# Performance work log

Hardware: AMD Instinct MI355X
Metric: run time of the kernel (lower is better)

## Reference

```python
import jax, jax.numpy as jnp
import numpy as np

RES = 200        # self.res, hard-coded in the module
MODES_OUT = 16
MODES_IN = 32
T_SEQ = 10
D_MODEL = 256
BATCH = 16


def setup_inputs() -> dict:
    key = jax.random.key(0)
    k1, k2, k3 = jax.random.split(key, 3)
    v = jax.random.normal(k1, (BATCH, T_SEQ, D_MODEL, 2, MODES_IN), dtype=jnp.float32)
    scale = 1.0 / (MODES_IN * MODES_OUT)
    # weights1 = scale * rand(T,1,1,mo,mi) cfloat; singleton dims broadcast -> store as [T,mo,mi]
    w_real = scale * jax.random.uniform(k2, (T_SEQ, MODES_OUT, MODES_IN), dtype=jnp.float32)
    w_imag = scale * jax.random.uniform(k3, (T_SEQ, MODES_OUT, MODES_IN), dtype=jnp.float32)
    return {"v": v, "w_real": w_real, "w_imag": w_imag}


def reference(v, w_real, w_imag):
    # v: [B,T,H,2,mi] -> complex x_ft = r + i*1j
    r = v[:, :, :, 0, :]  # [B,T,H,mi]
    i = v[:, :, :, 1, :]
    # einsum 'bthix,thiox->bthox' with h=i=1 in weights == broadcast complex multiply
    wr = w_real[None, :, None, :, :]  # [1,T,1,mo,mi]
    wi = w_imag[None, :, None, :, :]
    rr = r[:, :, :, None, :]          # [B,T,H,1,mi]
    ii = i[:, :, :, None, :]
    re = rr * wr - ii * wi            # [B,T,H,mo,mi] = Re(out_ft)
    im = rr * wi + ii * wr            # Im(out_ft)
    amp = jax.nn.relu(jnp.sqrt(re * re + im * im))  # relu(|out_ft|)
    ph = jnp.arctan2(im, re)                          # angle(out_ft)
    # cosine reconstruction grid: theta[o,x] = 2*pi*f_o*x, f from fftfreq(res, d=1/(res-1))
    x_res = jnp.linspace(0.0, 1.0, RES).astype(jnp.float32)
    dx = x_res[1] - x_res[0]
    freqs = jnp.fft.fftfreq(RES, d=dx)[:MODES_OUT].astype(jnp.float32)  # [mo]
    theta = (2.0 * jnp.pi) * freqs[:, None] * x_res[None, :]            # [mo,res]
    # sum over mi of amp*cos(theta + ph) = cos(theta)*sum(amp*cos ph) - sin(theta)*sum(amp*sin ph)
    # (exact trig identity; avoids materializing the 6-D [B,T,H,mo,mi,res] tensor)
    C = jnp.sum(amp * jnp.cos(ph), axis=-1)  # [B,T,H,mo]
    S = jnp.sum(amp * jnp.sin(ph), axis=-1)  # [B,T,H,mo]
    out = (jnp.einsum('btho,ox->btxh', C, jnp.cos(theta))
           - jnp.einsum('btho,ox->btxh', S, jnp.sin(theta)))  # [B,T,res,H]
    return out
```

## Files before the change

kernel.cpp:

```cpp
#include <hip/hip_runtime.h>

#define B_   16
#define T_   10
#define D_   256
#define MI_  32
#define MO_  16
#define RES_ 200
#define TWO_PI 6.28318530717958647692f

#define HSLICE 32
#define NHS    (D_ / HSLICE)
#define VPAD   68
#define BT_STRIDE (2 * MO_ * D_)

using f32x4 = __attribute__((ext_vector_type(4))) float;
using v2f   = __attribute__((ext_vector_type(2))) float;

__global__ __launch_bounds__(256) void spectral_cs(
    const float* __restrict__ v,
    const float* __restrict__ w_real,
    const float* __restrict__ w_imag,
    float* __restrict__ ws)
{
    const int a    = blockIdx.x;
    const int r    = a & 7;
    const int rest = a >> 3;
    const int hs   = rest & 7;
    const int q    = rest >> 3;
    const int bt   = 8 * q + r;
    const int t    = bt % T_;

    __shared__ float s_v[HSLICE * VPAD];

    {
        const float4* gv = reinterpret_cast<const float4*>(
            v + ((size_t)bt * D_ + hs * HSLICE) * (2 * MI_));
        #pragma unroll
        for (int j = 0; j < 2; ++j) {
            const int f = threadIdx.x + 256 * j;
            const int h = f >> 4;
            const int m = (f & 15) * 4;
            *reinterpret_cast<float4*>(&s_v[h * VPAD + m]) = gv[f];
        }
    }
    __syncthreads();

    const int og  = threadIdx.x >> 5;
    const int h_l = threadIdx.x & 31;
    const int o0  = og * 2;
    const int h_g = hs * HSLICE + h_l;

    float rr[MI_], ii[MI_];
    #pragma unroll
    for (int j = 0; j < 8; ++j) {
        float4 q4 = *reinterpret_cast<const float4*>(&s_v[h_l * VPAD + 4 * j]);
        rr[4*j+0]=q4.x; rr[4*j+1]=q4.y; rr[4*j+2]=q4.z; rr[4*j+3]=q4.w;
    }
    #pragma unroll
    for (int j = 0; j < 8; ++j) {
        float4 q4 = *reinterpret_cast<const float4*>(&s_v[h_l * VPAD + 32 + 4 * j]);
        ii[4*j+0]=q4.x; ii[4*j+1]=q4.y; ii[4*j+2]=q4.z; ii[4*j+3]=q4.w;
    }

    const float* wrt = w_real + ((size_t)t * MO_ + o0) * MI_;
    const float* wit = w_imag + ((size_t)t * MO_ + o0) * MI_;

    float* wsb = ws + (size_t)bt * BT_STRIDE;
    #pragma unroll
    for (int ol = 0; ol < 2; ++ol) {
        const float4* wa = reinterpret_cast<const float4*>(wrt + ol * MI_);
        const float4* wb = reinterpret_cast<const float4*>(wit + ol * MI_);
        float c = 0.f, s = 0.f;
        #pragma unroll
        for (int mq = 0; mq < 8; ++mq) {
            float4 a4 = wa[mq];
            float4 b4 = wb[mq];
            c = fmaf(rr[4*mq+0], a4.x, c); c = fmaf(-ii[4*mq+0], b4.x, c);
            s = fmaf(rr[4*mq+0], b4.x, s); s = fmaf( ii[4*mq+0], a4.x, s);
            c = fmaf(rr[4*mq+1], a4.y, c); c = fmaf(-ii[4*mq+1], b4.y, c);
            s = fmaf(rr[4*mq+1], b4.y, s); s = fmaf( ii[4*mq+1], a4.y, s);
            c = fmaf(rr[4*mq+2], a4.z, c); c = fmaf(-ii[4*mq+2], b4.z, c);
            s = fmaf(rr[4*mq+2], b4.z, s); s = fmaf( ii[4*mq+2], a4.z, s);
            c = fmaf(rr[4*mq+3], a4.w, c); c = fmaf(-ii[4*mq+3], b4.w, c);
            s = fmaf(rr[4*mq+3], b4.w, s); s = fmaf( ii[4*mq+3], a4.w, s);
        }
        const int o = o0 + ol;
        v2f p; p.x = c; p.y = s;
        *reinterpret_cast<v2f*>(&wsb[2 * (o * D_ + h_g)]) = p;
    }
}

__global__ __launch_bounds__(256) void spectral_ift(
    const float* __restrict__ ws,
    float* __restrict__ out)
{
    const int b    = blockIdx.x;
    const int r    = b & 7;
    const int rest = b >> 3;
    const int qb   = rest & 3;
    const int q    = rest >> 2;
    const int bt   = 8 * q + r;
    const int wave = threadIdx.x >> 6;
    const int lane = threadIdx.x & 63;
    const int g    = qb * 4 + wave;
    const int h0   = lane * 4;

    __shared__ float s_cs[BT_STRIDE];

    {
        const float4* g4 = reinterpret_cast<const float4*>(
            ws + (size_t)bt * BT_STRIDE);
        float4* s4 = reinterpret_cast<float4*>(s_cs);
        #pragma unroll
        for (int i = 0; i < 8; ++i)
            s4[threadIdx.x + 256 * i] = g4[threadIdx.x + 256 * i];
    }
    __syncthreads();

    v2f CS0[MO_], CS1[MO_], CS2[MO_], CS3[MO_];
    #pragma unroll
    for (int o = 0; o < MO_; ++o) {
        float4 q0 = *reinterpret_cast<const float4*>(&s_cs[2 * (o * D_ + h0)]);
        float4 q1 = *reinterpret_cast<const float4*>(&s_cs[2 * (o * D_ + h0) + 4]);
        CS0[o].x = q0.x; CS0[o].y = q0.y;
        CS1[o].x = q0.z; CS1[o].y = q0.w;
        CS2[o].x = q1.x; CS2[o].y = q1.y;
        CS3[o].x = q1.z; CS3[o].y = q1.w;
    }

    float* ob = out + (size_t)bt * RES_ * D_;

    #pragma unroll
    for (int k = 0; k < 7; ++k) {
        const int s = g + 16 * k;
        if (s <= 100) {
            const float phi = (float)s * (TWO_PI / (float)RES_);
            float s1, c1;
            __sincosf(phi, &s1, &c1);

            v2f ab0 = {0.f, 0.f}, ab1 = {0.f, 0.f};
            v2f ab2 = {0.f, 0.f}, ab3 = {0.f, 0.f};
            v2f cs;  cs.x = 1.f; cs.y = 0.f;
            #pragma unroll
            for (int o = 0; o < MO_; ++o) {
                ab0 = __builtin_elementwise_fma(CS0[o], cs, ab0);
                ab1 = __builtin_elementwise_fma(CS1[o], cs, ab1);
                ab2 = __builtin_elementwise_fma(CS2[o], cs, ab2);
                ab3 = __builtin_elementwise_fma(CS3[o], cs, ab3);
                const float nc = fmaf(cs.x, c1, -(cs.y * s1));
                const float ns = fmaf(cs.y, c1,  (cs.x * s1));
                cs.x = nc; cs.y = ns;
            }

            const int mr = (s == 0) ? 0 : (RES_ - s);
            f32x4 lo, hi;
            lo.x = ab0.x - ab0.y; hi.x = ab0.x + ab0.y;
            lo.y = ab1.x - ab1.y; hi.y = ab1.x + ab1.y;
            lo.z = ab2.x - ab2.y; hi.z = ab2.x + ab2.y;
            lo.w = ab3.x - ab3.y; hi.w = ab3.x + ab3.y;
            __builtin_nontemporal_store(
                lo, reinterpret_cast<f32x4*>(&ob[(size_t)s  * D_ + h0]));
            __builtin_nontemporal_store(
                hi, reinterpret_cast<f32x4*>(&ob[(size_t)mr * D_ + h0]));
        }
    }
}

extern "C" void kernel_launch(void* const* d_in, const int* in_sizes, int n_in,
                              void* d_out, int out_size, void* d_ws, size_t ws_size,
                              hipStream_t stream) {
    const float* v  = (const float*)d_in[0];
    const float* wr = (const float*)d_in[1];
    const float* wi = (const float*)d_in[2];
    float* out = (float*)d_out;
    float* ws  = (float*)d_ws;

    spectral_cs <<<B_ * T_ * NHS, 256, 0, stream>>>(v, wr, wi, ws);
    spectral_ift<<<B_ * T_ * 4,   256, 0, stream>>>(ws, out);
}
```

Baseline: 21.65 us.

## Double ift block size, halve per-thread columns, split rotation recurrence into even/odd chains

The inverse-transform kernel now runs 512 threads per block, and each thread covers 2 hidden columns instead of 4. This halves the per-thread register arrays, which should allow higher occupancy. The twiddle recurrence is split into two interleaved chains that step by 2*phi, which shortens the serial dependency chain of the rotations. In exchange the global stores shrink from 16-byte to 8-byte vectors, and the rotation arithmetic is repeated per thread for fewer outputs.

```diff
diff --git a/kernel.cpp b/kernel.cpp
--- a/kernel.cpp
+++ b/kernel.cpp
@@ -90,7 +90,7 @@
     }
 }
 
-__global__ __launch_bounds__(256) void spectral_ift(
+__global__ __launch_bounds__(512, 4) void spectral_ift(
     const float* __restrict__ ws,
     float* __restrict__ out)
 {
@@ -102,8 +102,9 @@
     const int bt   = 8 * q + r;
     const int wave = threadIdx.x >> 6;
     const int lane = threadIdx.x & 63;
-    const int g    = qb * 4 + wave;
-    const int h0   = lane * 4;
+    const int strm = qb * 4 + (wave >> 1);
+    const int half = wave & 1;
+    const int h0   = half * 128 + lane * 2;
 
     __shared__ float s_cs[BT_STRIDE];
 
@@ -112,56 +113,56 @@
             ws + (size_t)bt * BT_STRIDE);
         float4* s4 = reinterpret_cast<float4*>(s_cs);
         #pragma unroll
-        for (int i = 0; i < 8; ++i)
-            s4[threadIdx.x + 256 * i] = g4[threadIdx.x + 256 * i];
+        for (int i = 0; i < 4; ++i)
+            s4[threadIdx.x + 512 * i] = g4[threadIdx.x + 512 * i];
     }
     __syncthreads();
 
-    v2f CS0[MO_], CS1[MO_], CS2[MO_], CS3[MO_];
+    v2f CS0[MO_], CS1[MO_];
     #pragma unroll
     for (int o = 0; o < MO_; ++o) {
-        float4 q0 = *reinterpret_cast<const float4*>(&s_cs[2 * (o * D_ + h0)]);
-        float4 q1 = *reinterpret_cast<const float4*>(&s_cs[2 * (o * D_ + h0) + 4]);
-        CS0[o].x = q0.x; CS0[o].y = q0.y;
-        CS1[o].x = q0.z; CS1[o].y = q0.w;
-        CS2[o].x = q1.x; CS2[o].y = q1.y;
-        CS3[o].x = q1.z; CS3[o].y = q1.w;
+        float4 q4 = *reinterpret_cast<const float4*>(&s_cs[2 * (o * D_ + h0)]);
+        CS0[o].x = q4.x; CS0[o].y = q4.y;
+        CS1[o].x = q4.z; CS1[o].y = q4.w;
     }
 
-    float* ob = out + (size_t)bt * RES_ * D_;
+    float* ob = out + (size_t)bt * RES_ * D_ + h0;
 
     #pragma unroll
     for (int k = 0; k < 7; ++k) {
-        const int s = g + 16 * k;
+        const int s = strm + 16 * k;
         if (s <= 100) {
             const float phi = (float)s * (TWO_PI / (float)RES_);
             float s1, c1;
             __sincosf(phi, &s1, &c1);
+            const float c2 = fmaf(c1, c1, -(s1 * s1));
+            const float s2 = 2.0f * c1 * s1;
 
             v2f ab0 = {0.f, 0.f}, ab1 = {0.f, 0.f};
-            v2f ab2 = {0.f, 0.f}, ab3 = {0.f, 0.f};
-            v2f cs;  cs.x = 1.f; cs.y = 0.f;
+            v2f ce;  ce.x = 1.f; ce.y = 0.f;
+            v2f co_; co_.x = c1; co_.y = s1;
             #pragma unroll
-            for (int o = 0; o < MO_; ++o) {
-                ab0 = __builtin_elementwise_fma(CS0[o], cs, ab0);
-                ab1 = __builtin_elementwise_fma(CS1[o], cs, ab1);
-                ab2 = __builtin_elementwise_fma(CS2[o], cs, ab2);
-                ab3 = __builtin_elementwise_fma(CS3[o], cs, ab3);
-                const float nc = fmaf(cs.x, c1, -(cs.y * s1));
-                const float ns = fmaf(cs.y, c1,  (cs.x * s1));
-                cs.x = nc; cs.y = ns;
+            for (int j = 0; j < MO_ / 2; ++j) {
+                ab0 = __builtin_elementwise_fma(CS0[2*j],     ce,  ab0);
+                ab1 = __builtin_elementwise_fma(CS1[2*j],     ce,  ab1);
+                ab0 = __builtin_elementwise_fma(CS0[2*j + 1], co_, ab0);
+                ab1 = __builtin_elementwise_fma(CS1[2*j + 1], co_, ab1);
+                const float ne_c = fmaf(ce.x,  c2, -(ce.y  * s2));
+                const float ne_s = fmaf(ce.y,  c2,  (ce.x  * s2));
+                const float no_c = fmaf(co_.x, c2, -(co_.y * s2));
+                const float no_s = fmaf(co_.y, c2,  (co_.x * s2));
+                ce.x = ne_c; ce.y = ne_s;
+                co_.x = no_c; co_.y = no_s;
             }
 
             const int mr = (s == 0) ? 0 : (RES_ - s);
-            f32x4 lo, hi;
-            lo.x = ab0.x - ab0.y; hi.x = ab0.x + ab0.y;
-            lo.y = ab1.x - ab1.y; hi.y = ab1.x + ab1.y;
-            lo.z = ab2.x - ab2.y; hi.z = ab2.x + ab2.y;
-            lo.w = ab3.x - ab3.y; hi.w = ab3.x + ab3.y;
+            v2f lo, hi;
+            lo.x = ab0.x - ab0.y; lo.y = ab1.x - ab1.y;
+            hi.x = ab0.x + ab0.y; hi.y = ab1.x + ab1.y;
             __builtin_nontemporal_store(
-                lo, reinterpret_cast<f32x4*>(&ob[(size_t)s  * D_ + h0]));
+                lo, reinterpret_cast<v2f*>(&ob[(size_t)s  * D_]));
             __builtin_nontemporal_store(
-                hi, reinterpret_cast<f32x4*>(&ob[(size_t)mr * D_ + h0]));
+                hi, reinterpret_cast<v2f*>(&ob[(size_t)mr * D_]));
         }
     }
 }
@@ -176,5 +177,5 @@
     float* ws  = (float*)d_ws;
 
     spectral_cs <<<B_ * T_ * NHS, 256, 0, stream>>>(v, wr, wi, ws);
-    spectral_ift<<<B_ * T_ * 4,   256, 0, stream>>>(ws, out);
+    spectral_ift<<<B_ * T_ * 4,   512, 0, stream>>>(ws, out);
 }
```

Result: slower. 22.24 us (+2.7%).
